# Performance work log

Measured on AMD Instinct MI355X. Metric: run time of the kernel, lower is better.

The kernel has to match this reference:

```python
import jax, jax.numpy as jnp
import numpy as np

B, T, C, H = 8, 2048, 1024, 128  # batch, seq, embed_dim, head_size

def setup_inputs() -> dict:
    key = jax.random.key(0)
    kx, kk, kq, kv = jax.random.split(key, 4)
    s = 1.0 / np.sqrt(C)  # ~nn.Linear init scale
    return {
        "x": jax.random.normal(kx, (B, T, C), dtype=jnp.float32),
        "Wk": jax.random.normal(kk, (H, C), dtype=jnp.float32) * s,
        "Wq": jax.random.normal(kq, (H, C), dtype=jnp.float32) * s,
        "Wv": jax.random.normal(kv, (H, C), dtype=jnp.float32) * s,
    }

def reference(x, Wk, Wq, Wv):
    b, t, c = x.shape
    # Faithful to source: q uses the KEY projection (bug in original); Wq is unused.
    k = jnp.einsum('btc,hc->bth', x, Wk)   # [B,T,H]
    q = jnp.einsum('btc,hc->bth', x, Wk)   # [B,T,H]  (self.key used for q)
    v = jnp.einsum('btc,hc->bth', x, Wv)   # [B,T,H]
    score = jnp.einsum('bqh,bkh->bqk', q, k) * (c ** -0.5)  # scale by C, per source
    causal = jnp.tril(jnp.ones((t, t), dtype=bool))
    score = jnp.where(causal, score, -jnp.inf)
    attn = jax.nn.softmax(score, axis=-1)   # [B,T,T]
    out = jnp.einsum('bqk,bkh->bqh', attn, v)  # [B,T,H]
    return out
```

## Files before the change

### kernel.cpp

```cpp
#include <hip/hip_runtime.h>
#include <hip/hip_bf16.h>

#define BATCH 8
#define SEQ   2048
#define EMB   1024
#define HD    128

typedef __attribute__((ext_vector_type(8))) short bf16x8;
typedef __attribute__((ext_vector_type(4))) float f32x4;

__device__ __forceinline__ short f2bf(float f) {
    union { float f; unsigned u; } v; v.f = f;
    unsigned r = v.u + 0x7fffu + ((v.u >> 16) & 1u);
    return (short)(r >> 16);
}


__global__ void prep_w(const float* __restrict__ Wk, const float* __restrict__ Wv,
                       short* __restrict__ Wimg) {
    int g  = blockIdx.x * 256 + threadIdx.x;
    int q  = g & 3;
    int l  = (g >> 2) & 15;
    int f  = (g >> 6) & 7;
    int kk = (g >> 9) & 1;
    int kc = (g >> 10) & 15;
    int nh = (g >> 14) & 1;
    const float* src = (nh ? Wv : Wk) + (size_t)(f * 16 + l) * EMB + kc * 64 + kk * 32 + q * 8;
    float4 f0 = *(const float4*)src;
    float4 f1 = *(const float4*)(src + 4);
    bf16x8 v;
    v[0]=f2bf(f0.x); v[1]=f2bf(f0.y); v[2]=f2bf(f0.z); v[3]=f2bf(f0.w);
    v[4]=f2bf(f1.x); v[5]=f2bf(f1.y); v[6]=f2bf(f1.z); v[7]=f2bf(f1.w);
    *(bf16x8*)&Wimg[(size_t)g * 8] = v;
}

__global__ __launch_bounds__(256, 2)
void proj_kernel(const float* __restrict__ x, const short* __restrict__ Wimg,
                 short* __restrict__ Kimg,
                 short* __restrict__ Vimg)
{
    __shared__ __align__(16) union {
        struct { short A[2][64][72]; short B[2][8192]; } st;
        short ep[8192];
    } sm;

    const int tid  = threadIdx.x;
    const int wave = tid >> 6;
    const int lane = tid & 63;
    const int quad = lane >> 4;
    const int l16  = lane & 15;
    const int nh   = blockIdx.x & 1;
    const int mt   = blockIdx.x >> 1;
    const int row0 = mt * 64;

    const int srow = tid >> 2;
    const int sseg = tid & 3;
    const float* xsrc = x + (size_t)(row0 + srow) * EMB + sseg * 16;
    const short* wsrc = Wimg + (size_t)nh * 131072;

    f32x4 acc[4][2];
#pragma unroll
    for (int a = 0; a < 4; ++a)
#pragma unroll
        for (int c = 0; c < 2; ++c) acc[a][c] = f32x4{0.f, 0.f, 0.f, 0.f};

    {
        float4 xv[4];
#pragma unroll
        for (int e = 0; e < 4; ++e) xv[e] = *(const float4*)(xsrc + e * 4);
#pragma unroll
        for (int i = 0; i < 4; ++i)
            *(bf16x8*)&sm.st.B[0][tid * 32 + i * 8] = *(const bf16x8*)&wsrc[tid * 32 + i * 8];
        bf16x8 v0, v1;
        v0[0]=f2bf(xv[0].x); v0[1]=f2bf(xv[0].y); v0[2]=f2bf(xv[0].z); v0[3]=f2bf(xv[0].w);
        v0[4]=f2bf(xv[1].x); v0[5]=f2bf(xv[1].y); v0[6]=f2bf(xv[1].z); v0[7]=f2bf(xv[1].w);
        v1[0]=f2bf(xv[2].x); v1[1]=f2bf(xv[2].y); v1[2]=f2bf(xv[2].z); v1[3]=f2bf(xv[2].w);
        v1[4]=f2bf(xv[3].x); v1[5]=f2bf(xv[3].y); v1[6]=f2bf(xv[3].z); v1[7]=f2bf(xv[3].w);
        *(bf16x8*)&sm.st.A[0][srow][sseg * 16]     = v0;
        *(bf16x8*)&sm.st.A[0][srow][sseg * 16 + 8] = v1;
    }
    __syncthreads();

    for (int kc = 0; kc < 16; ++kc) {
        const int cur = kc & 1, nxt = cur ^ 1;
        float4 xv[4];
        bf16x8 wl[4];
        if (kc < 15) {
            const float* nx = xsrc + (kc + 1) * 64;
#pragma unroll
            for (int e = 0; e < 4; ++e) xv[e] = *(const float4*)(nx + e * 4);
            const short* nw = wsrc + (size_t)(kc + 1) * 8192;
#pragma unroll
            for (int i = 0; i < 4; ++i) wl[i] = *(const bf16x8*)&nw[tid * 32 + i * 8];
        }

#pragma unroll
        for (int kk = 0; kk < 2; ++kk) {
            bf16x8 bfr[2];
#pragma unroll
            for (int f2 = 0; f2 < 2; ++f2)
                bfr[f2] = *(const bf16x8*)&sm.st.B[cur][(((kk * 8 + wave * 2 + f2) * 16 + l16) * 4 + quad) * 8];
#pragma unroll
            for (int mf = 0; mf < 4; ++mf) {
                bf16x8 af = *(const bf16x8*)&sm.st.A[cur][mf * 16 + l16][kk * 32 + quad * 8];
#pragma unroll
                for (int f2 = 0; f2 < 2; ++f2)
                    acc[mf][f2] = __builtin_amdgcn_mfma_f32_16x16x32_bf16(af, bfr[f2], acc[mf][f2], 0, 0, 0);
            }
        }

        if (kc < 15) {
#pragma unroll
            for (int i = 0; i < 4; ++i)
                *(bf16x8*)&sm.st.B[nxt][tid * 32 + i * 8] = wl[i];
            bf16x8 v0, v1;
            v0[0]=f2bf(xv[0].x); v0[1]=f2bf(xv[0].y); v0[2]=f2bf(xv[0].z); v0[3]=f2bf(xv[0].w);
            v0[4]=f2bf(xv[1].x); v0[5]=f2bf(xv[1].y); v0[6]=f2bf(xv[1].z); v0[7]=f2bf(xv[1].w);
            v1[0]=f2bf(xv[2].x); v1[1]=f2bf(xv[2].y); v1[2]=f2bf(xv[2].z); v1[3]=f2bf(xv[2].w);
            v1[4]=f2bf(xv[3].x); v1[5]=f2bf(xv[3].y); v1[6]=f2bf(xv[3].z); v1[7]=f2bf(xv[3].w);
            *(bf16x8*)&sm.st.A[nxt][srow][sseg * 16]     = v0;
            *(bf16x8*)&sm.st.A[nxt][srow][sseg * 16 + 8] = v1;
        }
        __syncthreads();
    }

#pragma unroll
    for (int mf = 0; mf < 4; ++mf)
#pragma unroll
        for (int f2 = 0; f2 < 2; ++f2)
#pragma unroll
            for (int r = 0; r < 4; ++r) {
                const int row = mf * 16 + quad * 4 + r;
                const int h   = wave * 32 + f2 * 16 + l16;
                int idx;
                if (nh == 0)
                    idx = ((((h >> 5) * 4 + (row >> 4)) * 16 + (row & 15)) * 4 + ((h >> 3) & 3)) * 8 + (h & 7);
                else
                    idx = ((((row >> 5) * 8 + (h >> 4)) * 16 + (h & 15)) * 4 + ((row >> 3) & 3)) * 8 + (row & 7);
                sm.ep[idx] = f2bf(acc[mf][f2][r]);
            }
    __syncthreads();

    {
        short* dst = (nh == 0 ? Kimg : Vimg) + (size_t)mt * 8192 + tid * 32;
#pragma unroll
        for (int i = 0; i < 4; ++i)
            *(bf16x8*)(dst + i * 8) = *(const bf16x8*)&sm.ep[tid * 32 + i * 8];
    }
}

#define LOG2E 1.4426950408889634f

__global__ __launch_bounds__(256, 2)
void attn_kernel(const short* __restrict__ Kimg,
                 const short* __restrict__ Vimg,
                 float* __restrict__ out)
{
    __shared__ __align__(16) short ps[4][1024];
    __shared__ float obuf[2][16][132];
    __shared__ float lbuf[2][16];

    const int tid  = threadIdx.x;
    const int wave = tid >> 6;
    const int lane = tid & 63;
    const int quad = lane >> 4;
    const int l16  = lane & 15;

    const int b    = blockIdx.x & 7;
    const int g    = blockIdx.x >> 3;
    const int pair = wave >> 1;
    const int p    = wave & 1;
    const int qt   = pair ? (127 - g) : g;
    const int n    = (qt >> 2) + 1;

    const short* Kb = Kimg + (size_t)b * 32 * 8192;
    const short* Vb = Vimg + (size_t)b * 32 * 8192;

    bf16x8 qf[4];
    {
        const short* qi = Kb + (size_t)(qt >> 2) * 8192;
        const int jsq = qt & 3;
#pragma unroll
        for (int kc = 0; kc < 4; ++kc)
            qf[kc] = *(const bf16x8*)&qi[(((kc * 4 + jsq) * 16 + l16) * 4 + quad) * 8];
    }

    f32x4 O[8];
#pragma unroll
    for (int f = 0; f < 8; ++f) O[f] = f32x4{0.f, 0.f, 0.f, 0.f};
    float lp[4] = {0.f, 0.f, 0.f, 0.f};

    const float coef = LOG2E * 0.03125f;
    short* psw = ps[wave];

    for (int jt = p; jt < n; jt += 2) {
        const short* ki = Kb + (size_t)jt * 8192;
        const short* vi = Vb + (size_t)jt * 8192;

        bf16x8 kfr[16];
#pragma unroll
        for (int kc = 0; kc < 4; ++kc)
#pragma unroll
            for (int js = 0; js < 4; ++js)
                kfr[kc * 4 + js] = *(const bf16x8*)&ki[(((kc * 4 + js) * 16 + l16) * 4 + quad) * 8];

        f32x4 S[4];
#pragma unroll
        for (int js = 0; js < 4; ++js) S[js] = f32x4{0.f, 0.f, 0.f, 0.f};
#pragma unroll
        for (int kc = 0; kc < 4; ++kc)
#pragma unroll
            for (int js = 0; js < 4; ++js)
                S[js] = __builtin_amdgcn_mfma_f32_16x16x32_bf16(qf[kc], kfr[kc * 4 + js], S[js], 0, 0, 0);

        bf16x8 vfr[16];
#pragma unroll
        for (int jc = 0; jc < 2; ++jc)
#pragma unroll
            for (int f = 0; f < 8; ++f)
                vfr[jc * 8 + f] = *(const bf16x8*)&vi[(((jc * 8 + f) * 16 + l16) * 4 + quad) * 8];

        const bool diag = (jt == n - 1);
#pragma unroll
        for (int js = 0; js < 4; ++js) {
            const int jj = jt * 64 + js * 16 + l16;
            const int cb = js * 2 + (l16 >> 3);
            const int e  = l16 & 7;
#pragma unroll
            for (int r = 0; r < 4; ++r) {
                float vv = S[js][r] * coef;
                if (diag && (jj > qt * 16 + quad * 4 + r)) vv = -INFINITY;
                float pe = exp2f(vv);
                lp[r] += pe;
                const int i8 = quad * 4 + r;
                psw[(i8 * 8 + (cb ^ (i8 & 7))) * 8 + e] = f2bf(pe);
            }
        }

#pragma unroll
        for (int jc = 0; jc < 2; ++jc) {
            const int pblk = l16 * 8 + ((jc * 4 + quad) ^ (l16 & 7));
            bf16x8 pa = *(const bf16x8*)&psw[pblk * 8];
#pragma unroll
            for (int f = 0; f < 8; ++f)
                O[f] = __builtin_amdgcn_mfma_f32_16x16x32_bf16(pa, vfr[jc * 8 + f], O[f], 0, 0, 0);
        }
    }

#pragma unroll
    for (int r = 0; r < 4; ++r) {
        float s = lp[r];
        s += __shfl_xor(s, 1);
        s += __shfl_xor(s, 2);
        s += __shfl_xor(s, 4);
        s += __shfl_xor(s, 8);
        lp[r] = s;
    }

    if (p == 1) {
#pragma unroll
        for (int f = 0; f < 8; ++f)
#pragma unroll
            for (int r = 0; r < 4; ++r)
                obuf[pair][quad * 4 + r][f * 16 + l16] = O[f][r];
        if (l16 == 0) {
#pragma unroll
            for (int r = 0; r < 4; ++r) lbuf[pair][quad * 4 + r] = lp[r];
        }
    }
    __syncthreads();

    if (p == 0) {
#pragma unroll
        for (int r = 0; r < 4; ++r) {
            const int row16 = quad * 4 + r;
            const float L   = lp[r] + lbuf[pair][row16];
            const float inv = 1.f / L;
            const int row   = qt * 16 + row16;
            float* dst = out + (size_t)(b * SEQ + row) * HD + l16;
#pragma unroll
            for (int f = 0; f < 8; ++f)
                dst[f * 16] = (O[f][r] + obuf[pair][row16][f * 16 + l16]) * inv;
        }
    }
}

extern "C" void kernel_launch(void* const* d_in, const int* in_sizes, int n_in,
                              void* d_out, int out_size, void* d_ws, size_t ws_size,
                              hipStream_t stream) {
    const float* x  = (const float*)d_in[0];
    const float* Wk = (const float*)d_in[1];
    const float* Wv = (const float*)d_in[3];
    float* out = (float*)d_out;

    short* Wimg = (short*)d_ws;
    short* Kimg = Wimg + (size_t)262144;
    short* Vimg = Kimg + (size_t)BATCH * 32 * 8192;

    prep_w<<<128, 256, 0, stream>>>(Wk, Wv, Wimg);
    proj_kernel<<<512, 256, 0, stream>>>(x, Wimg, Kimg, Vimg);
    attn_kernel<<<512, 256, 0, stream>>>(Kimg, Vimg, out);
}
```

Measured before the change: 158.0 us.

## Fuse K/V projection per block and split attention KV loop across four waves

The projection kernel now runs 512 threads per block and computes both K and V for a 64-row tile. Each x tile is therefore loaded and converted to bf16 once instead of twice, and W fragments are read straight from global memory instead of being staged in LDS. The attention kernel gives each block a single 16-row query tile with four waves splitting the KV tiles, and doubles the grid. Partial outputs are merged with LDS atomics, and K/V fragment loads are split into phases to cut register use toward four blocks per CU. The trade-offs are extra LDS atomic traffic, direct global W reads, and more blocks with uneven per-wave work on short query tiles.

```diff
diff --git a/kernel.cpp b/kernel.cpp
--- a/kernel.cpp
+++ b/kernel.cpp
@@ -34,14 +34,14 @@
     *(bf16x8*)&Wimg[(size_t)g * 8] = v;
 }
 
-__global__ __launch_bounds__(256, 2)
+__global__ __launch_bounds__(512, 2)
 void proj_kernel(const float* __restrict__ x, const short* __restrict__ Wimg,
                  short* __restrict__ Kimg,
                  short* __restrict__ Vimg)
 {
     __shared__ __align__(16) union {
-        struct { short A[2][64][72]; short B[2][8192]; } st;
-        short ep[8192];
+        short A[2][64][72];
+        short ep[16384];
     } sm;
 
     const int tid  = threadIdx.x;
@@ -49,13 +49,13 @@
     const int lane = tid & 63;
     const int quad = lane >> 4;
     const int l16  = lane & 15;
-    const int nh   = blockIdx.x & 1;
-    const int mt   = blockIdx.x >> 1;
+    const int nh   = wave >> 2;
+    const int fb   = (wave & 3) * 2;
+    const int mt   = blockIdx.x;
     const int row0 = mt * 64;
 
-    const int srow = tid >> 2;
-    const int sseg = tid & 3;
-    const float* xsrc = x + (size_t)(row0 + srow) * EMB + sseg * 16;
+    const int srow = tid >> 3, sseg = tid & 7;
+    const float* xsrc = x + (size_t)(row0 + srow) * EMB + sseg * 8;
     const short* wsrc = Wimg + (size_t)nh * 131072;
 
     f32x4 acc[4][2];
@@ -65,61 +65,46 @@
         for (int c = 0; c < 2; ++c) acc[a][c] = f32x4{0.f, 0.f, 0.f, 0.f};
 
     {
-        float4 xv[4];
-#pragma unroll
-        for (int e = 0; e < 4; ++e) xv[e] = *(const float4*)(xsrc + e * 4);
-#pragma unroll
-        for (int i = 0; i < 4; ++i)
-            *(bf16x8*)&sm.st.B[0][tid * 32 + i * 8] = *(const bf16x8*)&wsrc[tid * 32 + i * 8];
-        bf16x8 v0, v1;
-        v0[0]=f2bf(xv[0].x); v0[1]=f2bf(xv[0].y); v0[2]=f2bf(xv[0].z); v0[3]=f2bf(xv[0].w);
-        v0[4]=f2bf(xv[1].x); v0[5]=f2bf(xv[1].y); v0[6]=f2bf(xv[1].z); v0[7]=f2bf(xv[1].w);
-        v1[0]=f2bf(xv[2].x); v1[1]=f2bf(xv[2].y); v1[2]=f2bf(xv[2].z); v1[3]=f2bf(xv[2].w);
-        v1[4]=f2bf(xv[3].x); v1[5]=f2bf(xv[3].y); v1[6]=f2bf(xv[3].z); v1[7]=f2bf(xv[3].w);
-        *(bf16x8*)&sm.st.A[0][srow][sseg * 16]     = v0;
-        *(bf16x8*)&sm.st.A[0][srow][sseg * 16 + 8] = v1;
+        float4 a0 = *(const float4*)xsrc;
+        float4 a1 = *(const float4*)(xsrc + 4);
+        bf16x8 v;
+        v[0]=f2bf(a0.x); v[1]=f2bf(a0.y); v[2]=f2bf(a0.z); v[3]=f2bf(a0.w);
+        v[4]=f2bf(a1.x); v[5]=f2bf(a1.y); v[6]=f2bf(a1.z); v[7]=f2bf(a1.w);
+        *(bf16x8*)&sm.A[0][srow][sseg * 8] = v;
     }
     __syncthreads();
 
     for (int kc = 0; kc < 16; ++kc) {
-        const int cur = kc & 1, nxt = cur ^ 1;
-        float4 xv[4];
-        bf16x8 wl[4];
+        const int cur = kc & 1;
+        float4 a0, a1;
         if (kc < 15) {
             const float* nx = xsrc + (kc + 1) * 64;
-#pragma unroll
-            for (int e = 0; e < 4; ++e) xv[e] = *(const float4*)(nx + e * 4);
-            const short* nw = wsrc + (size_t)(kc + 1) * 8192;
-#pragma unroll
-            for (int i = 0; i < 4; ++i) wl[i] = *(const bf16x8*)&nw[tid * 32 + i * 8];
-        }
-
-#pragma unroll
-        for (int kk = 0; kk < 2; ++kk) {
-            bf16x8 bfr[2];
+            a0 = *(const float4*)nx;
+            a1 = *(const float4*)(nx + 4);
+        }
+        const short* wc = wsrc + (size_t)kc * 8192;
+        bf16x8 bfr[2][2];
+#pragma unroll
+        for (int kk = 0; kk < 2; ++kk)
 #pragma unroll
             for (int f2 = 0; f2 < 2; ++f2)
-                bfr[f2] = *(const bf16x8*)&sm.st.B[cur][(((kk * 8 + wave * 2 + f2) * 16 + l16) * 4 + quad) * 8];
+                bfr[kk][f2] = *(const bf16x8*)&wc[(((kk * 8 + fb + f2) * 16 + l16) * 4 + quad) * 8];
+
+#pragma unroll
+        for (int kk = 0; kk < 2; ++kk)
 #pragma unroll
             for (int mf = 0; mf < 4; ++mf) {
-                bf16x8 af = *(const bf16x8*)&sm.st.A[cur][mf * 16 + l16][kk * 32 + quad * 8];
+                bf16x8 af = *(const bf16x8*)&sm.A[cur][mf * 16 + l16][kk * 32 + quad * 8];
 #pragma unroll
                 for (int f2 = 0; f2 < 2; ++f2)
-                    acc[mf][f2] = __builtin_amdgcn_mfma_f32_16x16x32_bf16(af, bfr[f2], acc[mf][f2], 0, 0, 0);
+                    acc[mf][f2] = __builtin_amdgcn_mfma_f32_16x16x32_bf16(af, bfr[kk][f2], acc[mf][f2], 0, 0, 0);
             }
-        }
 
         if (kc < 15) {
-#pragma unroll
-            for (int i = 0; i < 4; ++i)
-                *(bf16x8*)&sm.st.B[nxt][tid * 32 + i * 8] = wl[i];
-            bf16x8 v0, v1;
-            v0[0]=f2bf(xv[0].x); v0[1]=f2bf(xv[0].y); v0[2]=f2bf(xv[0].z); v0[3]=f2bf(xv[0].w);
-            v0[4]=f2bf(xv[1].x); v0[5]=f2bf(xv[1].y); v0[6]=f2bf(xv[1].z); v0[7]=f2bf(xv[1].w);
-            v1[0]=f2bf(xv[2].x); v1[1]=f2bf(xv[2].y); v1[2]=f2bf(xv[2].z); v1[3]=f2bf(xv[2].w);
-            v1[4]=f2bf(xv[3].x); v1[5]=f2bf(xv[3].y); v1[6]=f2bf(xv[3].z); v1[7]=f2bf(xv[3].w);
-            *(bf16x8*)&sm.st.A[nxt][srow][sseg * 16]     = v0;
-            *(bf16x8*)&sm.st.A[nxt][srow][sseg * 16 + 8] = v1;
+            bf16x8 v;
+            v[0]=f2bf(a0.x); v[1]=f2bf(a0.y); v[2]=f2bf(a0.z); v[3]=f2bf(a0.w);
+            v[4]=f2bf(a1.x); v[5]=f2bf(a1.y); v[6]=f2bf(a1.z); v[7]=f2bf(a1.w);
+            *(bf16x8*)&sm.A[cur ^ 1][srow][sseg * 8] = v;
         }
         __syncthreads();
     }
@@ -131,34 +116,37 @@
 #pragma unroll
             for (int r = 0; r < 4; ++r) {
                 const int row = mf * 16 + quad * 4 + r;
-                const int h   = wave * 32 + f2 * 16 + l16;
+                const int h   = (fb + f2) * 16 + l16;
                 int idx;
                 if (nh == 0)
                     idx = ((((h >> 5) * 4 + (row >> 4)) * 16 + (row & 15)) * 4 + ((h >> 3) & 3)) * 8 + (h & 7);
                 else
-                    idx = ((((row >> 5) * 8 + (h >> 4)) * 16 + (h & 15)) * 4 + ((row >> 3) & 3)) * 8 + (row & 7);
+                    idx = 8192 + ((((row >> 5) * 8 + (h >> 4)) * 16 + (h & 15)) * 4 + ((row >> 3) & 3)) * 8 + (row & 7);
                 sm.ep[idx] = f2bf(acc[mf][f2][r]);
             }
     __syncthreads();
 
     {
-        short* dst = (nh == 0 ? Kimg : Vimg) + (size_t)mt * 8192 + tid * 32;
-#pragma unroll
-        for (int i = 0; i < 4; ++i)
-            *(bf16x8*)(dst + i * 8) = *(const bf16x8*)&sm.ep[tid * 32 + i * 8];
+#pragma unroll
+        for (int i = 0; i < 4; ++i) {
+            const int g = i * 512 + tid;
+            short* dst = (g < 1024) ? (Kimg + (size_t)mt * 8192 + g * 8)
+                                    : (Vimg + (size_t)mt * 8192 + (g - 1024) * 8);
+            *(bf16x8*)dst = *(const bf16x8*)&sm.ep[g * 8];
+        }
     }
 }
 
 #define LOG2E 1.4426950408889634f
 
-__global__ __launch_bounds__(256, 2)
+__global__ __launch_bounds__(256, 4)
 void attn_kernel(const short* __restrict__ Kimg,
                  const short* __restrict__ Vimg,
                  float* __restrict__ out)
 {
     __shared__ __align__(16) short ps[4][1024];
-    __shared__ float obuf[2][16][132];
-    __shared__ float lbuf[2][16];
+    __shared__ float obuf[16][132];
+    __shared__ float lbuf[4][16];
 
     const int tid  = threadIdx.x;
     const int wave = tid >> 6;
@@ -166,12 +154,12 @@
     const int quad = lane >> 4;
     const int l16  = lane & 15;
 
-    const int b    = blockIdx.x & 7;
-    const int g    = blockIdx.x >> 3;
-    const int pair = wave >> 1;
-    const int p    = wave & 1;
-    const int qt   = pair ? (127 - g) : g;
-    const int n    = (qt >> 2) + 1;
+    const int b  = blockIdx.x & 7;
+    const int u  = blockIdx.x >> 3;
+    const int qt = (u & 1) ? (127 - (u >> 1)) : (u >> 1);
+    const int n  = (qt >> 2) + 1;
+
+    for (int i = tid; i < 16 * 132; i += 256) ((float*)obuf)[i] = 0.f;
 
     const short* Kb = Kimg + (size_t)b * 32 * 8192;
     const short* Vb = Vimg + (size_t)b * 32 * 8192;
@@ -193,32 +181,32 @@
     const float coef = LOG2E * 0.03125f;
     short* psw = ps[wave];
 
-    for (int jt = p; jt < n; jt += 2) {
+    for (int jt = wave; jt < n; jt += 4) {
         const short* ki = Kb + (size_t)jt * 8192;
         const short* vi = Vb + (size_t)jt * 8192;
 
-        bf16x8 kfr[16];
-#pragma unroll
-        for (int kc = 0; kc < 4; ++kc)
-#pragma unroll
-            for (int js = 0; js < 4; ++js)
-                kfr[kc * 4 + js] = *(const bf16x8*)&ki[(((kc * 4 + js) * 16 + l16) * 4 + quad) * 8];
-
         f32x4 S[4];
 #pragma unroll
         for (int js = 0; js < 4; ++js) S[js] = f32x4{0.f, 0.f, 0.f, 0.f};
 #pragma unroll
-        for (int kc = 0; kc < 4; ++kc)
-#pragma unroll
-            for (int js = 0; js < 4; ++js)
-                S[js] = __builtin_amdgcn_mfma_f32_16x16x32_bf16(qf[kc], kfr[kc * 4 + js], S[js], 0, 0, 0);
-
-        bf16x8 vfr[16];
-#pragma unroll
-        for (int jc = 0; jc < 2; ++jc)
-#pragma unroll
-            for (int f = 0; f < 8; ++f)
-                vfr[jc * 8 + f] = *(const bf16x8*)&vi[(((jc * 8 + f) * 16 + l16) * 4 + quad) * 8];
+        for (int ph = 0; ph < 2; ++ph) {
+            bf16x8 kfr[8];
+#pragma unroll
+            for (int kc = 0; kc < 2; ++kc)
+#pragma unroll
+                for (int js = 0; js < 4; ++js)
+                    kfr[kc * 4 + js] = *(const bf16x8*)&ki[((((ph * 2 + kc) * 4 + js) * 16 + l16) * 4 + quad) * 8];
+#pragma unroll
+            for (int kc = 0; kc < 2; ++kc)
+#pragma unroll
+                for (int js = 0; js < 4; ++js)
+                    S[js] = __builtin_amdgcn_mfma_f32_16x16x32_bf16(qf[ph * 2 + kc], kfr[kc * 4 + js], S[js], 0, 0, 0);
+        }
+
+        bf16x8 vfr[8];
+#pragma unroll
+        for (int f = 0; f < 8; ++f)
+            vfr[f] = *(const bf16x8*)&vi[((f * 16 + l16) * 4 + quad) * 8];
 
         const bool diag = (jt == n - 1);
 #pragma unroll
@@ -237,13 +225,21 @@
             }
         }
 
-#pragma unroll
-        for (int jc = 0; jc < 2; ++jc) {
-            const int pblk = l16 * 8 + ((jc * 4 + quad) ^ (l16 & 7));
+        {
+            const int pblk = l16 * 8 + (quad ^ (l16 & 7));
             bf16x8 pa = *(const bf16x8*)&psw[pblk * 8];
+            bf16x8 vf1[8];
 #pragma unroll
             for (int f = 0; f < 8; ++f)
-                O[f] = __builtin_amdgcn_mfma_f32_16x16x32_bf16(pa, vfr[jc * 8 + f], O[f], 0, 0, 0);
+                vf1[f] = *(const bf16x8*)&vi[(((8 + f) * 16 + l16) * 4 + quad) * 8];
+#pragma unroll
+            for (int f = 0; f < 8; ++f)
+                O[f] = __builtin_amdgcn_mfma_f32_16x16x32_bf16(pa, vfr[f], O[f], 0, 0, 0);
+            const int pblk1 = l16 * 8 + ((4 + quad) ^ (l16 & 7));
+            bf16x8 pa1 = *(const bf16x8*)&psw[pblk1 * 8];
+#pragma unroll
+            for (int f = 0; f < 8; ++f)
+                O[f] = __builtin_amdgcn_mfma_f32_16x16x32_bf16(pa1, vf1[f], O[f], 0, 0, 0);
         }
     }
 
@@ -256,32 +252,27 @@
         s += __shfl_xor(s, 8);
         lp[r] = s;
     }
-
-    if (p == 1) {
-#pragma unroll
-        for (int f = 0; f < 8; ++f)
-#pragma unroll
-            for (int r = 0; r < 4; ++r)
-                obuf[pair][quad * 4 + r][f * 16 + l16] = O[f][r];
-        if (l16 == 0) {
-#pragma unroll
-            for (int r = 0; r < 4; ++r) lbuf[pair][quad * 4 + r] = lp[r];
-        }
-    }
-    __syncthreads();
-
-    if (p == 0) {
-#pragma unroll
-        for (int r = 0; r < 4; ++r) {
-            const int row16 = quad * 4 + r;
-            const float L   = lp[r] + lbuf[pair][row16];
-            const float inv = 1.f / L;
-            const int row   = qt * 16 + row16;
-            float* dst = out + (size_t)(b * SEQ + row) * HD + l16;
-#pragma unroll
-            for (int f = 0; f < 8; ++f)
-                dst[f * 16] = (O[f][r] + obuf[pair][row16][f * 16 + l16]) * inv;
-        }
+    if (l16 == 0) {
+#pragma unroll
+        for (int r = 0; r < 4; ++r) lbuf[wave][quad * 4 + r] = lp[r];
+    }
+    __syncthreads();
+
+#pragma unroll
+    for (int f = 0; f < 8; ++f)
+#pragma unroll
+        for (int r = 0; r < 4; ++r)
+            atomicAdd(&obuf[quad * 4 + r][f * 16 + l16], O[f][r]);
+    __syncthreads();
+
+    {
+        const int row = tid >> 4;
+        const int c8  = (tid & 15) * 8;
+        const float L = lbuf[0][row] + lbuf[1][row] + lbuf[2][row] + lbuf[3][row];
+        const float inv = 1.f / L;
+        float* dst = out + (size_t)(b * SEQ + qt * 16 + row) * HD + c8;
+#pragma unroll
+        for (int uu = 0; uu < 8; ++uu) dst[uu] = obuf[row][c8 + uu] * inv;
     }
 }
 
@@ -298,6 +289,6 @@
     short* Vimg = Kimg + (size_t)BATCH * 32 * 8192;
 
     prep_w<<<128, 256, 0, stream>>>(Wk, Wv, Wimg);
-    proj_kernel<<<512, 256, 0, stream>>>(x, Wimg, Kimg, Vimg);
-    attn_kernel<<<512, 256, 0, stream>>>(Kimg, Vimg, out);
-}
+    proj_kernel<<<256, 512, 0, stream>>>(x, Wimg, Kimg, Vimg);
+    attn_kernel<<<1024, 256, 0, stream>>>(Kimg, Vimg, out);
+}
```

Measured after the change: 212.3 us. 1.34x slower.
